# Kernel tuning notes

Hardware: AMD Instinct MI355X
Metric: run time of the kernel (lower is better)

## Reference

```python
import jax, jax.numpy as jnp
import numpy as np

N, IN_DIM, OUT_DIM = 8192, 512, 256
ALPHA = 0.2
NEG_INF = -9e15


def setup_inputs() -> dict:
    key = jax.random.key(0)
    k1, k2, k3, k4 = jax.random.split(key, 4)
    node_features = jax.random.normal(k1, (N, IN_DIM), dtype=jnp.float32)
    adj_matrix = jax.random.randint(k2, (N, N), 0, 2, dtype=jnp.int32)
    # xavier-uniform linear weight [out,in] -> store as [in,out]
    lim_w = float(np.sqrt(6.0 / (IN_DIM + OUT_DIM)))
    W = jax.random.uniform(k3, (IN_DIM, OUT_DIM), dtype=jnp.float32, minval=-lim_w, maxval=lim_w)
    b = jnp.zeros((OUT_DIM,), dtype=jnp.float32)
    # attention Linear(2*out_dim, 1): weight a [2*out_dim], bias scalar
    lim_a = float(np.sqrt(6.0 / (2 * OUT_DIM + 1)))
    a = jax.random.uniform(k4, (2 * OUT_DIM,), dtype=jnp.float32, minval=-lim_a, maxval=lim_a)
    a_bias = jnp.zeros((), dtype=jnp.float32)
    return {"adj_matrix": adj_matrix, "node_features": node_features, "W": W, "b": b, "a": a, "a_bias": a_bias}


def reference(adj_matrix, node_features, W, b, a, a_bias):
    # h = Linear(node_features); dropout is identity in eval mode
    h = node_features @ W + b                     # [N, D]
    # attention(cat(h_i, h_j)) == h_i @ a_l + h_j @ a_r + a_bias
    a_l, a_r = a[:OUT_DIM], a[OUT_DIM:]
    e_l = h @ a_l                                 # [N]
    e_r = h @ a_r                                 # [N]
    e = jax.nn.leaky_relu(e_l[:, None] + e_r[None, :] + a_bias, ALPHA)  # [N, N]
    scores = jnp.where(adj_matrix > 0, e, NEG_INF)
    attention = jax.nn.softmax(scores, axis=1)    # [N, N]
    h_prime = attention @ h                       # [N, D]
    return h_prime
```

## Files before the change

### kernel.cpp

```cpp
#include <hip/hip_runtime.h>

#define N 8192
#define DIN 512
#define DOUT 256
#define ALPHA 0.2f
#define NEG_INF -9.0e15f

typedef __attribute__((ext_vector_type(8))) short bf16x8;
typedef __attribute__((ext_vector_type(4))) float f32x4;
typedef __attribute__((ext_vector_type(4))) int   i32x4;

__device__ __forceinline__ unsigned f2bf_u(float f) {
    unsigned u = __builtin_bit_cast(unsigned, f);
    return (u + 0x7fffu + ((u >> 16) & 1u)) >> 16;
}
__device__ __forceinline__ unsigned pack2bf(float lo, float hi) {
    return f2bf_u(lo) | (f2bf_u(hi) << 16);
}
union U4BF8 { uint4 u; bf16x8 v; };

__device__ __forceinline__ void async_copy16(const ushort* g, ushort* l) {
    __builtin_amdgcn_global_load_lds(
        (const __attribute__((address_space(1))) unsigned*)g,
        (__attribute__((address_space(3))) unsigned*)l, 16, 0, 0);
}

__global__ __launch_bounds__(256) void wb_kernel(const float* __restrict__ W,
                                                 ushort* __restrict__ WB) {
    const int g = blockIdx.x * 256 + threadIdx.x;
    const int c = g & 255, k8 = g >> 8;
    const float* wp = W + (size_t)(k8 * 8) * DOUT + c;
    U4BF8 o;
    o.u.x = pack2bf(wp[0 * DOUT], wp[1 * DOUT]);
    o.u.y = pack2bf(wp[2 * DOUT], wp[3 * DOUT]);
    o.u.z = pack2bf(wp[4 * DOUT], wp[5 * DOUT]);
    o.u.w = pack2bf(wp[6 * DOUT], wp[7 * DOUT]);
    *(uint4*)(WB + (size_t)g * 8) = o.u;
}

__global__ __launch_bounds__(256) void h_kernel(
        const float* __restrict__ X, const ushort* __restrict__ WB,
        const float* __restrict__ bvec, const float* __restrict__ a,
        ushort* __restrict__ hB, float* __restrict__ el, float* __restrict__ er)
{
    __shared__ float red[4][64][65];
    __shared__ float elr[2][4][16];
    const int t = threadIdx.x;
    const int w = t >> 6, l = t & 63, q = l >> 4, n = l & 15;
    const int i0 = blockIdx.x * 16;
    f32x4 acc[16];
    #pragma unroll
    for (int ct = 0; ct < 16; ++ct) acc[ct] = (f32x4){0.f, 0.f, 0.f, 0.f};
    const float* xp = X + (size_t)(i0 + n) * DIN + q * 8;

    #pragma unroll
    for (int ks = 0; ks < 4; ++ks) {
        const int k0 = w * 128 + ks * 32;
        const float4 x0 = *(const float4*)(xp + k0);
        const float4 x1 = *(const float4*)(xp + k0 + 4);
        U4BF8 pa;
        pa.u.x = pack2bf(x0.x, x0.y); pa.u.y = pack2bf(x0.z, x0.w);
        pa.u.z = pack2bf(x1.x, x1.y); pa.u.w = pack2bf(x1.z, x1.w);
        const ushort* wbp = WB + ((k0 >> 3) + q) * 2048 + n * 8;
        bf16x8 bfr[16];
        #pragma unroll
        for (int ct = 0; ct < 16; ++ct) bfr[ct] = *(const bf16x8*)(wbp + ct * 128);
        #pragma unroll
        for (int ct = 0; ct < 16; ++ct)
            acc[ct] = __builtin_amdgcn_mfma_f32_16x16x32_bf16(pa.v, bfr[ct], acc[ct], 0, 0, 0);
    }
    #pragma unroll
    for (int ct = 0; ct < 16; ++ct)
        #pragma unroll
        for (int r = 0; r < 4; ++r) red[w][l][ct * 4 + r] = acc[ct][r];
    __syncthreads();

    float pl[4] = {0.f, 0.f, 0.f, 0.f}, pr[4] = {0.f, 0.f, 0.f, 0.f};
    const int hbase = (blockIdx.x * 2 + (q >> 1)) * 2048 + n * 8 + (q & 1) * 4;
    #pragma unroll
    for (int c2 = 0; c2 < 4; ++c2) {
        const int ct = w * 4 + c2;
        const float bb = bvec[ct * 16 + n];
        const float al = a[ct * 16 + n];
        const float ar = a[DOUT + ct * 16 + n];
        float v[4];
        #pragma unroll
        for (int r = 0; r < 4; ++r) {
            v[r] = red[0][l][ct * 4 + r] + red[1][l][ct * 4 + r]
                 + red[2][l][ct * 4 + r] + red[3][l][ct * 4 + r] + bb;
            pl[r] += v[r] * al;
            pr[r] += v[r] * ar;
        }
        ushort4 hp;
        hp.x = (ushort)f2bf_u(v[0]); hp.y = (ushort)f2bf_u(v[1]);
        hp.z = (ushort)f2bf_u(v[2]); hp.w = (ushort)f2bf_u(v[3]);
        *(ushort4*)&hB[hbase + ct * 128] = hp;
    }
    #pragma unroll
    for (int r = 0; r < 4; ++r) {
        #pragma unroll
        for (int off = 1; off < 16; off <<= 1) {
            pl[r] += __shfl_xor(pl[r], off);
            pr[r] += __shfl_xor(pr[r], off);
        }
    }
    if (n == 0) {
        #pragma unroll
        for (int r = 0; r < 4; ++r) {
            elr[0][w][q * 4 + r] = pl[r];
            elr[1][w][q * 4 + r] = pr[r];
        }
    }
    __syncthreads();
    if (t < 16) {
        el[i0 + t] = elr[0][0][t] + elr[0][1][t] + elr[0][2][t] + elr[0][3][t];
        er[i0 + t] = elr[1][0][t] + elr[1][1][t] + elr[1][2][t] + elr[1][3][t];
    }
}

#define EXP8(ELM, E0, E1, M0, M1, PA, LS)                                          \
    {                                                                              \
        float v, p0, p1, p2, p3, p4, p5, p6, p7;                                   \
        v = ELM + E0.x; v = fmaxf(v, ALPHA * v); p0 = __expf(M0.x > 0 ? v : NEG_INF); \
        v = ELM + E0.y; v = fmaxf(v, ALPHA * v); p1 = __expf(M0.y > 0 ? v : NEG_INF); \
        v = ELM + E0.z; v = fmaxf(v, ALPHA * v); p2 = __expf(M0.z > 0 ? v : NEG_INF); \
        v = ELM + E0.w; v = fmaxf(v, ALPHA * v); p3 = __expf(M0.w > 0 ? v : NEG_INF); \
        v = ELM + E1.x; v = fmaxf(v, ALPHA * v); p4 = __expf(M1.x > 0 ? v : NEG_INF); \
        v = ELM + E1.y; v = fmaxf(v, ALPHA * v); p5 = __expf(M1.y > 0 ? v : NEG_INF); \
        v = ELM + E1.z; v = fmaxf(v, ALPHA * v); p6 = __expf(M1.z > 0 ? v : NEG_INF); \
        v = ELM + E1.w; v = fmaxf(v, ALPHA * v); p7 = __expf(M1.w > 0 ? v : NEG_INF); \
        LS += p0 + p1 + p2 + p3 + p4 + p5 + p6 + p7;                               \
        PA.u.x = pack2bf(p0, p1); PA.u.y = pack2bf(p2, p3);                        \
        PA.u.z = pack2bf(p4, p5); PA.u.w = pack2bf(p6, p7);                        \
    }

__global__ __launch_bounds__(512, 4) void attn_kernel(
        const int* __restrict__ adj, const float* __restrict__ el,
        const float* __restrict__ er, const float* __restrict__ ab,
        const ushort* __restrict__ hB, float* __restrict__ pout,
        float* __restrict__ plsum)
{
    __shared__ ushort stage[2][16384];
    __shared__ float ers[1024];
    const int t = threadIdx.x;
    const int w = t >> 6, l = t & 63, q = l >> 4, n = l & 15;
    const int rb = blockIdx.x >> 3, je = blockIdx.x & 7;
    const int j0 = je * 1024;
    const int row = rb * 128 + w * 16 + n;
    const float elm = el[row] + ab[0];
    const int* alp = adj + (size_t)row * N + j0 + q * 8;

    f32x4 acc[16];
    #pragma unroll
    for (int ct = 0; ct < 16; ++ct) acc[ct] = (f32x4){0.f, 0.f, 0.f, 0.f};
    float lsum = 0.f;

    if (t < 256) *(float4*)&ers[t * 4] = *(const float4*)&er[j0 + t * 4];
    i32x4 a[4];
    #pragma unroll
    for (int kg = 0; kg < 2; ++kg) {
        a[2 * kg]     = *(const i32x4*)(alp + kg * 32);
        a[2 * kg + 1] = *(const i32x4*)(alp + kg * 32 + 4);
    }
    {
        const ushort* g = hB + (size_t)j0 * 256 + t * 8;
        ushort* lb = &stage[0][t * 8];
        #pragma unroll
        for (int i = 0; i < 4; ++i) async_copy16(g + i * 4096, lb + i * 4096);
    }

    for (int s = 0; s < 16; ++s) {
        __syncthreads();
        if (s < 15) {
            const ushort* g = hB + (size_t)(j0 + (s + 1) * 64) * 256 + t * 8;
            ushort* lb = &stage[(s + 1) & 1][t * 8];
            #pragma unroll
            for (int i = 0; i < 4; ++i) async_copy16(g + i * 4096, lb + i * 4096);
        }
        U4BF8 pa[2];
        #pragma unroll
        for (int kg = 0; kg < 2; ++kg) {
            const float4 e0 = *(const float4*)&ers[s * 64 + kg * 32 + q * 8];
            const float4 e1 = *(const float4*)&ers[s * 64 + kg * 32 + q * 8 + 4];
            EXP8(elm, e0, e1, a[2 * kg], a[2 * kg + 1], pa[kg], lsum);
        }
        if (s < 15) {
            const int* ap = alp + (s + 1) * 64;
            #pragma unroll
            for (int kg = 0; kg < 2; ++kg) {
                a[2 * kg]     = *(const i32x4*)(ap + kg * 32);
                a[2 * kg + 1] = *(const i32x4*)(ap + kg * 32 + 4);
            }
        }
        #pragma unroll
        for (int kg = 0; kg < 2; ++kg) {
            const ushort* sb = &stage[s & 1][(kg * 4 + q) * 2048 + n * 8];
            #pragma unroll
            for (int ct = 0; ct < 16; ++ct) {
                const bf16x8 bf = *(const bf16x8*)(sb + ct * 128);
                acc[ct] = __builtin_amdgcn_mfma_f32_16x16x32_bf16(pa[kg].v, bf, acc[ct], 0, 0, 0);
            }
        }
    }

    lsum += __shfl_xor(lsum, 16);
    lsum += __shfl_xor(lsum, 32);
    if (l < 16) plsum[(size_t)je * N + row] = lsum;

    float* pb = pout + ((size_t)je * N + rb * 128 + w * 16 + q * 4) * 256 + n;
    #pragma unroll
    for (int ct = 0; ct < 16; ++ct)
        #pragma unroll
        for (int r = 0; r < 4; ++r)
            __builtin_nontemporal_store(acc[ct][r], pb + (size_t)r * 256 + ct * 16);
}

__global__ __launch_bounds__(256) void combine_kernel(
        const float* __restrict__ pout, const float* __restrict__ plsum,
        float* __restrict__ out)
{
    const int t = threadIdx.x;
    const int row = blockIdx.x * 4 + (t >> 6);
    const int c = (t & 63) * 4;
    const size_t idx = (size_t)row * 256 + c;
    const size_t qs = (size_t)N * 256;
    float4 acc = *(const float4*)&pout[idx];
    float ls = plsum[row];
    #pragma unroll
    for (int k = 1; k < 8; ++k) {
        const float4 v = *(const float4*)&pout[idx + k * qs];
        acc.x += v.x; acc.y += v.y; acc.z += v.z; acc.w += v.w;
        ls += plsum[k * N + row];
    }
    const float li = 1.0f / ls;
    float4 o;
    o.x = acc.x * li; o.y = acc.y * li; o.z = acc.z * li; o.w = acc.w * li;
    *(float4*)&out[idx] = o;
}

extern "C" void kernel_launch(void* const* d_in, const int* in_sizes, int n_in,
                              void* d_out, int out_size, void* d_ws, size_t ws_size,
                              hipStream_t stream) {
    const int*   adj = (const int*)  d_in[0];
    const float* X   = (const float*)d_in[1];
    const float* W   = (const float*)d_in[2];
    const float* b   = (const float*)d_in[3];
    const float* a   = (const float*)d_in[4];
    const float* ab  = (const float*)d_in[5];
    float* out = (float*)d_out;

    ushort* hB    = (ushort*)d_ws;
    ushort* WB    = hB + (size_t)N * DOUT;
    float*  el    = (float*)(WB + (size_t)DIN * DOUT);
    float*  er    = el + N;
    float*  plsum = er + N;
    float*  pout  = plsum + 8 * N;

    wb_kernel<<<dim3(64), dim3(256), 0, stream>>>(W, WB);
    h_kernel<<<dim3(N / 16), dim3(256), 0, stream>>>(X, WB, b, a, hB, el, er);
    attn_kernel<<<dim3(512), dim3(512), 0, stream>>>(adj, el, er, ab, hB, pout, plsum);
    combine_kernel<<<dim3(N / 4), dim3(256), 0, stream>>>(pout, plsum, out);
}
```

Measured before the change: 441.6 us.

## Switch attention matmul to 32x32x16 MFMA with split column halves

The attention kernel now uses 32x32x16 bf16 MFMA instead of 16x16x32. Each pair of waves shares a 32-row group, and each wave in the pair covers half of the 256 output columns, which cuts the accumulator count from 16 f32x4 to 4 f32x16. Exp/mask computation is split into two halves that are interleaved with the MFMA batches, and adjacency prefetch is split to match, to overlap VALU and matrix work. The trade-off is that each exp value is now computed redundantly by two waves, the two column-half waves duplicate the adjacency loads, and the output write pattern changes.

```diff
diff --git a/kernel.cpp b/kernel.cpp
--- a/kernel.cpp
+++ b/kernel.cpp
@@ -8,6 +8,7 @@
 
 typedef __attribute__((ext_vector_type(8))) short bf16x8;
 typedef __attribute__((ext_vector_type(4))) float f32x4;
+typedef __attribute__((ext_vector_type(16))) float f32x16;
 typedef __attribute__((ext_vector_type(4))) int   i32x4;
 
 __device__ __forceinline__ unsigned f2bf_u(float f) {
@@ -143,25 +144,28 @@
     __shared__ ushort stage[2][16384];
     __shared__ float ers[1024];
     const int t = threadIdx.x;
-    const int w = t >> 6, l = t & 63, q = l >> 4, n = l & 15;
+    const int w = t >> 6, l = t & 63;
+    const int rg = w >> 1, ch = w & 1;
+    const int r32 = l & 31, hi = l >> 5;
     const int rb = blockIdx.x >> 3, je = blockIdx.x & 7;
     const int j0 = je * 1024;
-    const int row = rb * 128 + w * 16 + n;
+    const int row = rb * 128 + rg * 32 + r32;
     const float elm = el[row] + ab[0];
-    const int* alp = adj + (size_t)row * N + j0 + q * 8;
-
-    f32x4 acc[16];
-    #pragma unroll
-    for (int ct = 0; ct < 16; ++ct) acc[ct] = (f32x4){0.f, 0.f, 0.f, 0.f};
+    const int* alp = adj + (size_t)row * N + j0 + hi * 8;
+
+    f32x16 acc[4];
+    #pragma unroll
+    for (int ct = 0; ct < 4; ++ct)
+        #pragma unroll
+        for (int r = 0; r < 16; ++r) acc[ct][r] = 0.f;
     float lsum = 0.f;
 
     if (t < 256) *(float4*)&ers[t * 4] = *(const float4*)&er[j0 + t * 4];
-    i32x4 a[4];
-    #pragma unroll
-    for (int kg = 0; kg < 2; ++kg) {
-        a[2 * kg]     = *(const i32x4*)(alp + kg * 32);
-        a[2 * kg + 1] = *(const i32x4*)(alp + kg * 32 + 4);
-    }
+    i32x4 adjA[4], adjB[4];
+    adjA[0] = *(const i32x4*)(alp +  0); adjA[1] = *(const i32x4*)(alp +  4);
+    adjA[2] = *(const i32x4*)(alp + 16); adjA[3] = *(const i32x4*)(alp + 20);
+    adjB[0] = *(const i32x4*)(alp + 32); adjB[1] = *(const i32x4*)(alp + 36);
+    adjB[2] = *(const i32x4*)(alp + 48); adjB[3] = *(const i32x4*)(alp + 52);
     {
         const ushort* g = hB + (size_t)j0 * 256 + t * 8;
         ushort* lb = &stage[0][t * 8];
@@ -177,42 +181,79 @@
             #pragma unroll
             for (int i = 0; i < 4; ++i) async_copy16(g + i * 4096, lb + i * 4096);
         }
-        U4BF8 pa[2];
-        #pragma unroll
-        for (int kg = 0; kg < 2; ++kg) {
-            const float4 e0 = *(const float4*)&ers[s * 64 + kg * 32 + q * 8];
-            const float4 e1 = *(const float4*)&ers[s * 64 + kg * 32 + q * 8 + 4];
-            EXP8(elm, e0, e1, a[2 * kg], a[2 * kg + 1], pa[kg], lsum);
+        const ushort* sbase = &stage[s & 1][ch * 1024 + r32 * 8];
+
+        U4BF8 pa0, pa1;
+        {
+            const float4 e00 = *(const float4*)&ers[s * 64 +  0 + hi * 8];
+            const float4 e01 = *(const float4*)&ers[s * 64 +  0 + hi * 8 + 4];
+            EXP8(elm, e00, e01, adjA[0], adjA[1], pa0, lsum);
+            const float4 e10 = *(const float4*)&ers[s * 64 + 16 + hi * 8];
+            const float4 e11 = *(const float4*)&ers[s * 64 + 16 + hi * 8 + 4];
+            EXP8(elm, e10, e11, adjA[2], adjA[3], pa1, lsum);
         }
         if (s < 15) {
             const int* ap = alp + (s + 1) * 64;
-            #pragma unroll
-            for (int kg = 0; kg < 2; ++kg) {
-                a[2 * kg]     = *(const i32x4*)(ap + kg * 32);
-                a[2 * kg + 1] = *(const i32x4*)(ap + kg * 32 + 4);
+            adjA[0] = *(const i32x4*)(ap +  0); adjA[1] = *(const i32x4*)(ap +  4);
+            adjA[2] = *(const i32x4*)(ap + 16); adjA[3] = *(const i32x4*)(ap + 20);
+        }
+        {
+            const ushort* sb0 = sbase + (0 + hi) * 2048;
+            const ushort* sb1 = sbase + (2 + hi) * 2048;
+            #pragma unroll
+            for (int ct = 0; ct < 4; ++ct) {
+                const bf16x8 bf = *(const bf16x8*)(sb0 + ct * 256);
+                acc[ct] = __builtin_amdgcn_mfma_f32_32x32x16_bf16(pa0.v, bf, acc[ct], 0, 0, 0);
             }
-        }
-        #pragma unroll
-        for (int kg = 0; kg < 2; ++kg) {
-            const ushort* sb = &stage[s & 1][(kg * 4 + q) * 2048 + n * 8];
-            #pragma unroll
-            for (int ct = 0; ct < 16; ++ct) {
-                const bf16x8 bf = *(const bf16x8*)(sb + ct * 128);
-                acc[ct] = __builtin_amdgcn_mfma_f32_16x16x32_bf16(pa[kg].v, bf, acc[ct], 0, 0, 0);
+            #pragma unroll
+            for (int ct = 0; ct < 4; ++ct) {
+                const bf16x8 bf = *(const bf16x8*)(sb1 + ct * 256);
+                acc[ct] = __builtin_amdgcn_mfma_f32_32x32x16_bf16(pa1.v, bf, acc[ct], 0, 0, 0);
             }
         }
-    }
-
-    lsum += __shfl_xor(lsum, 16);
+
+        U4BF8 pa2, pa3;
+        {
+            const float4 e20 = *(const float4*)&ers[s * 64 + 32 + hi * 8];
+            const float4 e21 = *(const float4*)&ers[s * 64 + 32 + hi * 8 + 4];
+            EXP8(elm, e20, e21, adjB[0], adjB[1], pa2, lsum);
+            const float4 e30 = *(const float4*)&ers[s * 64 + 48 + hi * 8];
+            const float4 e31 = *(const float4*)&ers[s * 64 + 48 + hi * 8 + 4];
+            EXP8(elm, e30, e31, adjB[2], adjB[3], pa3, lsum);
+        }
+        if (s < 15) {
+            const int* ap = alp + (s + 1) * 64;
+            adjB[0] = *(const i32x4*)(ap + 32); adjB[1] = *(const i32x4*)(ap + 36);
+            adjB[2] = *(const i32x4*)(ap + 48); adjB[3] = *(const i32x4*)(ap + 52);
+        }
+        {
+            const ushort* sb2 = sbase + (4 + hi) * 2048;
+            const ushort* sb3 = sbase + (6 + hi) * 2048;
+            #pragma unroll
+            for (int ct = 0; ct < 4; ++ct) {
+                const bf16x8 bf = *(const bf16x8*)(sb2 + ct * 256);
+                acc[ct] = __builtin_amdgcn_mfma_f32_32x32x16_bf16(pa2.v, bf, acc[ct], 0, 0, 0);
+            }
+            #pragma unroll
+            for (int ct = 0; ct < 4; ++ct) {
+                const bf16x8 bf = *(const bf16x8*)(sb3 + ct * 256);
+                acc[ct] = __builtin_amdgcn_mfma_f32_32x32x16_bf16(pa3.v, bf, acc[ct], 0, 0, 0);
+            }
+        }
+    }
+
     lsum += __shfl_xor(lsum, 32);
-    if (l < 16) plsum[(size_t)je * N + row] = lsum;
-
-    float* pb = pout + ((size_t)je * N + rb * 128 + w * 16 + q * 4) * 256 + n;
-    #pragma unroll
-    for (int ct = 0; ct < 16; ++ct)
-        #pragma unroll
-        for (int r = 0; r < 4; ++r)
-            __builtin_nontemporal_store(acc[ct][r], pb + (size_t)r * 256 + ct * 16);
+    if (ch == 0 && l < 32)
+        plsum[(size_t)je * N + rb * 128 + rg * 32 + l] = lsum;
+
+    float* pb = pout + ((size_t)je * N + rb * 128 + rg * 32) * 256 + ch * 128 + r32;
+    #pragma unroll
+    for (int ct = 0; ct < 4; ++ct)
+        #pragma unroll
+        for (int r = 0; r < 16; ++r) {
+            const int rl = (r & 3) + 8 * (r >> 2) + 4 * hi;
+            __builtin_nontemporal_store(acc[ct][r], pb + (size_t)rl * 256 + ct * 32);
+        }
 }
 
 __global__ __launch_bounds__(256) void combine_kernel(
```

Result: no change. 444.7 us (+0.7%).
